# Kernel optimization log

Measured on AMD Instinct MI355X. Metric: run time of the kernel, lower is better.

The kernel has to match this reference:

```python
import jax, jax.numpy as jnp
import numpy as np

N_USER = 60082   # n_fields: size of station/field table
N_STATION = 14695
D = 128
B = 8
K = 32


def setup_inputs() -> dict:
    key = jax.random.key(0)
    ks = jax.random.split(key, 20)
    inp = {
        'user_embedding': jax.random.normal(ks[0], (B, D), jnp.float32),
        'station_embedding': jax.random.normal(ks[1], (N_USER, D), jnp.float32),
        'raw_field_embed': jax.random.normal(ks[2], (N_USER, D), jnp.float32),
        'his_nodes': jax.random.randint(ks[3], (B, K), 0, N_USER),
        'now_nodes': jax.random.randint(ks[4], (B, K), 0, N_USER),
        'user_id': jax.random.randint(ks[5], (B,), 0, N_STATION),
        # learned parameters
        'user_emb_table': jax.random.normal(ks[6], (N_STATION, D), jnp.float32) * 0.02,
        'station_emb_table': jax.random.normal(ks[7], (N_USER, D), jnp.float32) * 0.02,
        'proj_w': jax.random.normal(ks[8], (D, D), jnp.float32) / np.sqrt(D),
        'proj_b': jnp.zeros((D,), jnp.float32),
        'theta': jax.random.uniform(ks[9], (N_STATION, 1), jnp.float32),
        'alpha': jax.random.uniform(ks[10], (N_USER, 1), jnp.float32),
        'w_his1': jax.random.normal(ks[11], (D, D // 2), jnp.float32) / np.sqrt(D),
        'b_his1': jnp.zeros((D // 2,), jnp.float32),
        'w_his2': jax.random.normal(ks[12], (D // 2, D), jnp.float32) / np.sqrt(D // 2),
        'b_his2': jnp.zeros((D,), jnp.float32),
        'w_st': jax.random.normal(ks[13], (D, 1), jnp.float32) / np.sqrt(D),
        'b_st': jnp.zeros((1,), jnp.float32),
        'w_u': jax.random.normal(ks[14], (D, 1), jnp.float32) / np.sqrt(D),
        'b_u': jnp.zeros((1,), jnp.float32),
    }
    return inp


def reference(user_embedding, station_embedding, raw_field_embed,
              user_emb_table, station_emb_table, proj_w, proj_b,
              theta, alpha, w_his1, b_his1, w_his2, b_his2,
              w_st, b_st, w_u, b_u,
              his_nodes, now_nodes, user_id):
    # user_mem_stat: gated mix of dynamic and static user embedding (dropout = eval identity)
    th = theta[user_id]                                    # [B,1]
    user_mem = (1.0 - th) * user_embedding + th * user_emb_table[user_id]  # [B,D]

    # full-table projection, shared across batch (the torch loop recomputes it)
    proj = station_emb_table @ proj_w + proj_b             # [N,D]

    b_idx = jnp.arange(B)[:, None]                         # [B,1]
    beta = jnp.zeros((B, N_USER), user_embedding.dtype)
    beta = beta.at[b_idx, now_nodes].set(1.0)
    beta = beta.at[b_idx, his_nodes].set(1.0)              # use_his=True path

    embed = (1.0 - beta[..., None] * alpha[None]) * proj[None]  # [B,N,D]

    # scatter-add current-node contribution
    now_add = alpha[now_nodes] * station_embedding[now_nodes]  # [B,K,D]
    embed = embed.at[b_idx, now_nodes].add(now_add)

    # history MLP (Linear -> LeakyReLU -> Linear) on gathered raw field embeds
    h = raw_field_embed[his_nodes]                         # [B,K,D]
    h = jax.nn.leaky_relu(h @ w_his1 + b_his1) @ w_his2 + b_his2
    embed = embed.at[b_idx, his_nodes].add(alpha[his_nodes] * h)

    station_out = (embed @ w_st)[..., 0] + b_st[0]         # [B,N]
    user_out = user_mem @ w_u + b_u                        # [B,1]
    return station_out + user_out                          # [B,N]
```

## Files before the change

### kernel.cpp

```cpp
#include <hip/hip_runtime.h>

#define NU 60082
#define NST 14695
#define D 128
#define B 8
#define K 32
#define NSTREAM ((NU + 63) / 64)

__global__ __launch_bounds__(256) void k_fused(
    const float* __restrict__ user_embedding,
    const float* __restrict__ station_embedding,
    const float* __restrict__ raw_field_embed,
    const int* __restrict__ his_nodes,
    const int* __restrict__ now_nodes,
    const int* __restrict__ user_id,
    const float* __restrict__ user_emb_table,
    const float* __restrict__ station_emb_table,
    const float* __restrict__ proj_w,
    const float* __restrict__ proj_b,
    const float* __restrict__ theta,
    const float* __restrict__ alpha,
    const float* __restrict__ w_his1,
    const float* __restrict__ b_his1,
    const float* __restrict__ w_his2,
    const float* __restrict__ b_his2,
    const float* __restrict__ w_st,
    const float* __restrict__ b_st,
    const float* __restrict__ w_u,
    const float* __restrict__ b_u,
    float* __restrict__ out)
{
    const int t = threadIdx.x;

    if (blockIdx.x < B) {
        __shared__ float s_wst[128];
        __shared__ float s_v[128];
        __shared__ float s_v2[64];
        __shared__ float s_rfe[32][128];
        __shared__ int   s_nodes[64];
        __shared__ float s_alpha[64];
        __shared__ float s_vals[64];
        __shared__ float s_sn[64];
        __shared__ float s_c, s_c2, s_uc;
        const int b = blockIdx.x;

        if (t < 32) ((float4*)s_wst)[t] = ((const float4*)w_st)[t];
        if (t >= 64 && t < 128) {
            int j = t - 64;
            s_nodes[j] = (j < K) ? now_nodes[b * K + j] : his_nodes[b * K + (j - K)];
        }
        __syncthreads();

        if (t < 128) {
            float acc = 0.f;
            const float4* pr = (const float4*)(proj_w + t * D);
            #pragma unroll 8
            for (int j = 0; j < 32; ++j) {
                float4 x = pr[j];
                float4 wv = ((float4*)s_wst)[j];
                acc += x.x * wv.x + x.y * wv.y + x.z * wv.z + x.w * wv.w;
            }
            s_v[t] = acc;
        } else if (t < 192) {
            int u = t - 128;
            float acc = 0.f;
            const float4* pr = (const float4*)(w_his2 + u * D);
            #pragma unroll 8
            for (int j = 0; j < 32; ++j) {
                float4 x = pr[j];
                float4 wv = ((float4*)s_wst)[j];
                acc += x.x * wv.x + x.y * wv.y + x.z * wv.z + x.w * wv.w;
            }
            s_v2[u] = acc;
        } else if (t < 224) {
            int l = t - 192;
            float4 x = ((const float4*)proj_b)[l];
            float4 wv = ((float4*)s_wst)[l];
            float p = x.x * wv.x + x.y * wv.y + x.z * wv.z + x.w * wv.w;
            #pragma unroll
            for (int off = 16; off >= 1; off >>= 1) p += __shfl_down(p, off, 32);
            if (l == 0) s_c = p;
        } else {
            int l = t - 224;
            float4 x = ((const float4*)b_his2)[l];
            float4 wv = ((float4*)s_wst)[l];
            float p = x.x * wv.x + x.y * wv.y + x.z * wv.z + x.w * wv.w;
            #pragma unroll
            for (int off = 16; off >= 1; off >>= 1) p += __shfl_down(p, off, 32);
            if (l == 0) s_c2 = p;
        }
        if (t < 32) {
            int uid = user_id[b];
            float th = theta[uid];
            float4 ue = ((const float4*)(user_embedding + b * D))[t];
            float4 ut = ((const float4*)(user_emb_table + (size_t)uid * D))[t];
            float4 wu = ((const float4*)w_u)[t];
            float p = ((1.f - th) * ue.x + th * ut.x) * wu.x
                    + ((1.f - th) * ue.y + th * ut.y) * wu.y
                    + ((1.f - th) * ue.z + th * ut.z) * wu.z
                    + ((1.f - th) * ue.w + th * ut.w) * wu.w;
            #pragma unroll
            for (int off = 16; off >= 1; off >>= 1) p += __shfl_down(p, off, 32);
            if (t == 0) s_uc = p + b_u[0] + b_st[0];
        }
        if (t >= 32 && t < 96) s_alpha[t - 32] = alpha[s_nodes[t - 32]];
        __syncthreads();

        {
            int j = t >> 3, c8 = t & 7;
            int n = s_nodes[32 + j];
            const float4* src = (const float4*)(raw_field_embed + (size_t)n * D);
            #pragma unroll
            for (int i = 0; i < 4; ++i)
                ((float4*)s_rfe[j])[c8 + 8 * i] = src[c8 + 8 * i];
        }
        __syncthreads();

        {
            const int u = t & 63, w = t >> 6;
            const float v2u = s_v2[u];
            const float bias = b_his1[u];
            float h1[8];
            #pragma unroll
            for (int j = 0; j < 8; ++j) h1[j] = bias;
            for (int dd = 0; dd < 128; dd += 8) {
                float wr[8];
                #pragma unroll
                for (int i = 0; i < 8; ++i) wr[i] = w_his1[(dd + i) * 64 + u];
                #pragma unroll
                for (int j = 0; j < 8; ++j) {
                    const float4* rf = (const float4*)&s_rfe[w * 8 + j][dd];
                    float4 a = rf[0], b4 = rf[1];
                    h1[j] += a.x * wr[0] + a.y * wr[1] + a.z * wr[2] + a.w * wr[3]
                           + b4.x * wr[4] + b4.y * wr[5] + b4.z * wr[6] + b4.w * wr[7];
                }
            }
            #pragma unroll
            for (int j = 0; j < 8; ++j) {
                float ha = h1[j] > 0.f ? h1[j] : 0.01f * h1[j];
                float val = ha * v2u;
                #pragma unroll
                for (int off = 32; off >= 1; off >>= 1) val += __shfl_down(val, off, 64);
                if (u == 0)
                    s_vals[32 + w * 8 + j] = s_alpha[32 + w * 8 + j] * (val + s_c2);
            }
        }
        {
            const int u = t & 63, w = t >> 6;
            #pragma unroll
            for (int r = 0; r < 8; ++r) {
                int j = w * 8 + r;
                int n = s_nodes[j];
                const float* se = station_embedding + (size_t)n * D;
                float p = se[u] * s_wst[u] + se[64 + u] * s_wst[64 + u];
                #pragma unroll
                for (int off = 32; off >= 1; off >>= 1) p += __shfl_down(p, off, 64);
                if (u == 0) s_vals[j] = s_alpha[j] * p;
            }
        }
        {
            int node = t >> 2, q = t & 3;
            const float4* sr = (const float4*)(station_emb_table + (size_t)s_nodes[node] * D);
            float p = 0.f;
            #pragma unroll
            for (int i = 0; i < 8; ++i) {
                float4 x = sr[q + 4 * i];
                float4 vv = ((float4*)s_v)[q + 4 * i];
                p += x.x * vv.x + x.y * vv.y + x.z * vv.z + x.w * vv.w;
            }
            p += __shfl_down(p, 2, 4);
            p += __shfl_down(p, 1, 4);
            if (q == 0) s_sn[node] = p + s_c;
        }
        __syncthreads();

        if (t < 64) {
            int n = s_nodes[t];
            bool first = true;
            for (int i = 0; i < t; ++i)
                if (s_nodes[i] == n) { first = false; break; }
            if (first) {
                float sum = 0.f;
                for (int i = 0; i < 64; ++i)
                    if (s_nodes[i] == n) sum += s_vals[i];
                out[(size_t)b * NU + n] = (1.f - s_alpha[t]) * s_sn[t] + s_uc + sum;
            }
        }
    } else {
        __shared__ float st_wst[128];
        __shared__ float st_v[128];
        __shared__ float st_tile[64];
        __shared__ float st_uc[8];
        __shared__ unsigned char st_flag[8 * 64];
        __shared__ float st_c;
        const int sb = blockIdx.x - B;
        const int row0 = sb * 64;

        if (t < 32) ((float4*)st_wst)[t] = ((const float4*)w_st)[t];
        if (t >= 128) ((int*)st_flag)[t - 128] = 0;
        __syncthreads();

        if (t < 128) {
            float acc = 0.f;
            const float4* pr = (const float4*)(proj_w + t * D);
            #pragma unroll 8
            for (int j = 0; j < 32; ++j) {
                float4 x = pr[j];
                float4 wv = ((float4*)st_wst)[j];
                acc += x.x * wv.x + x.y * wv.y + x.z * wv.z + x.w * wv.w;
            }
            st_v[t] = acc;
        } else if (t < 160) {
            int l = t - 128;
            float4 x = ((const float4*)proj_b)[l];
            float4 wv = ((float4*)st_wst)[l];
            float p = x.x * wv.x + x.y * wv.y + x.z * wv.z + x.w * wv.w;
            #pragma unroll
            for (int off = 16; off >= 1; off >>= 1) p += __shfl_down(p, off, 32);
            if (l == 0) st_c = p;
        }
        {
            int n0 = now_nodes[t];
            if ((n0 >> 6) == sb) st_flag[(t >> 5) * 64 + (n0 & 63)] = 1;
            int n1 = his_nodes[t];
            if ((n1 >> 6) == sb) st_flag[(t >> 5) * 64 + (n1 & 63)] = 1;
        }
        {
            int u = t >> 5, l = t & 31;
            int uid = user_id[u];
            float th = theta[uid];
            float4 ue = ((const float4*)(user_embedding + u * D))[l];
            float4 ut = ((const float4*)(user_emb_table + (size_t)uid * D))[l];
            float4 wu = ((const float4*)w_u)[l];
            float p = ((1.f - th) * ue.x + th * ut.x) * wu.x
                    + ((1.f - th) * ue.y + th * ut.y) * wu.y
                    + ((1.f - th) * ue.z + th * ut.z) * wu.z
                    + ((1.f - th) * ue.w + th * ut.w) * wu.w;
            #pragma unroll
            for (int off = 16; off >= 1; off >>= 1) p += __shfl_down(p, off, 32);
            if (l == 0) st_uc[u] = p + b_u[0] + b_st[0];
        }
        __syncthreads();

        const int w    = t >> 6;
        const int lane = t & 63;
        const int half = lane >> 5;
        const int l32  = lane & 31;
        const float4 vv = ((const float4*)st_v)[l32];
        const float  c  = st_c;
        #pragma unroll
        for (int i = 0; i < 8; ++i) {
            int r = i * 8 + w * 2 + half;
            int row = row0 + r;
            float acc = 0.f;
            if (row < NU) {
                float4 x = ((const float4*)(station_emb_table + (size_t)row * D))[l32];
                acc = x.x * vv.x + x.y * vv.y + x.z * vv.z + x.w * vv.w;
            }
            #pragma unroll
            for (int off = 16; off >= 1; off >>= 1) acc += __shfl_down(acc, off, 32);
            if (l32 == 0) st_tile[r] = acc + c;
        }
        __syncthreads();

        const int nl = t & 63;
        const int b0 = t >> 6;
        const int row = row0 + nl;
        if (row < NU) {
            float sv = st_tile[nl];
            if (!st_flag[b0 * 64 + nl])
                out[(size_t)b0 * NU + row] = sv + st_uc[b0];
            if (!st_flag[(b0 + 4) * 64 + nl])
                out[(size_t)(b0 + 4) * NU + row] = sv + st_uc[b0 + 4];
        }
    }
}

extern "C" void kernel_launch(void* const* d_in, const int* in_sizes, int n_in,
                              void* d_out, int out_size, void* d_ws, size_t ws_size,
                              hipStream_t stream) {
    const float* user_embedding    = (const float*)d_in[0];
    const float* station_embedding = (const float*)d_in[1];
    const float* raw_field_embed   = (const float*)d_in[2];
    const int*   his_nodes         = (const int*)d_in[3];
    const int*   now_nodes         = (const int*)d_in[4];
    const int*   user_id           = (const int*)d_in[5];
    const float* user_emb_table    = (const float*)d_in[6];
    const float* station_emb_table = (const float*)d_in[7];
    const float* proj_w            = (const float*)d_in[8];
    const float* proj_b            = (const float*)d_in[9];
    const float* theta             = (const float*)d_in[10];
    const float* alpha             = (const float*)d_in[11];
    const float* w_his1            = (const float*)d_in[12];
    const float* b_his1            = (const float*)d_in[13];
    const float* w_his2            = (const float*)d_in[14];
    const float* b_his2            = (const float*)d_in[15];
    const float* w_st              = (const float*)d_in[16];
    const float* b_st              = (const float*)d_in[17];
    const float* w_u               = (const float*)d_in[18];
    const float* b_u               = (const float*)d_in[19];
    float* out = (float*)d_out;

    hipLaunchKernelGGL(k_fused, dim3(B + NSTREAM), dim3(256), 0, stream,
                       user_embedding, station_embedding, raw_field_embed,
                       his_nodes, now_nodes, user_id, user_emb_table,
                       station_emb_table, proj_w, proj_b, theta, alpha,
                       w_his1, b_his1, w_his2, b_his2,
                       w_st, b_st, w_u, b_u, out);
}
```

Before: 166.3 us.

## Distribute sparse node corrections into owning row-tile blocks instead of per-batch blocks

Removes the eight dedicated per-batch blocks that handled the gathered now/his nodes. Each streaming tile block now collects, via shared-memory atomics, the node entries that fall in its 64-row range and computes their corrections locally, reusing the projected tile value already in shared memory. This removes the long serial critical path of the per-batch blocks (the MLP over 32 history rows), but adds a conditional tail to some tile blocks, redundant global reads of w_his1 per history node, and an extra barrier.

```diff
diff --git a/kernel.cpp b/kernel.cpp
--- a/kernel.cpp
+++ b/kernel.cpp
@@ -5,7 +5,7 @@
 #define D 128
 #define B 8
 #define K 32
-#define NSTREAM ((NU + 63) / 64)
+#define NBLK ((NU + 63) / 64)
 
 __global__ __launch_bounds__(256) void k_fused(
     const float* __restrict__ user_embedding,
@@ -30,248 +30,187 @@
     const float* __restrict__ b_u,
     float* __restrict__ out)
 {
-    const int t = threadIdx.x;
-
-    if (blockIdx.x < B) {
-        __shared__ float s_wst[128];
-        __shared__ float s_v[128];
-        __shared__ float s_v2[64];
-        __shared__ float s_rfe[32][128];
-        __shared__ int   s_nodes[64];
-        __shared__ float s_alpha[64];
-        __shared__ float s_vals[64];
-        __shared__ float s_sn[64];
-        __shared__ float s_c, s_c2, s_uc;
-        const int b = blockIdx.x;
-
-        if (t < 32) ((float4*)s_wst)[t] = ((const float4*)w_st)[t];
-        if (t >= 64 && t < 128) {
-            int j = t - 64;
-            s_nodes[j] = (j < K) ? now_nodes[b * K + j] : his_nodes[b * K + (j - K)];
-        }
-        __syncthreads();
-
-        if (t < 128) {
-            float acc = 0.f;
-            const float4* pr = (const float4*)(proj_w + t * D);
-            #pragma unroll 8
-            for (int j = 0; j < 32; ++j) {
-                float4 x = pr[j];
-                float4 wv = ((float4*)s_wst)[j];
-                acc += x.x * wv.x + x.y * wv.y + x.z * wv.z + x.w * wv.w;
-            }
-            s_v[t] = acc;
-        } else if (t < 192) {
-            int u = t - 128;
-            float acc = 0.f;
-            const float4* pr = (const float4*)(w_his2 + u * D);
-            #pragma unroll 8
-            for (int j = 0; j < 32; ++j) {
-                float4 x = pr[j];
-                float4 wv = ((float4*)s_wst)[j];
-                acc += x.x * wv.x + x.y * wv.y + x.z * wv.z + x.w * wv.w;
-            }
-            s_v2[u] = acc;
-        } else if (t < 224) {
-            int l = t - 192;
-            float4 x = ((const float4*)proj_b)[l];
-            float4 wv = ((float4*)s_wst)[l];
-            float p = x.x * wv.x + x.y * wv.y + x.z * wv.z + x.w * wv.w;
-            #pragma unroll
-            for (int off = 16; off >= 1; off >>= 1) p += __shfl_down(p, off, 32);
-            if (l == 0) s_c = p;
-        } else {
-            int l = t - 224;
-            float4 x = ((const float4*)b_his2)[l];
-            float4 wv = ((float4*)s_wst)[l];
-            float p = x.x * wv.x + x.y * wv.y + x.z * wv.z + x.w * wv.w;
-            #pragma unroll
-            for (int off = 16; off >= 1; off >>= 1) p += __shfl_down(p, off, 32);
-            if (l == 0) s_c2 = p;
-        }
-        if (t < 32) {
-            int uid = user_id[b];
-            float th = theta[uid];
-            float4 ue = ((const float4*)(user_embedding + b * D))[t];
-            float4 ut = ((const float4*)(user_emb_table + (size_t)uid * D))[t];
-            float4 wu = ((const float4*)w_u)[t];
-            float p = ((1.f - th) * ue.x + th * ut.x) * wu.x
-                    + ((1.f - th) * ue.y + th * ut.y) * wu.y
-                    + ((1.f - th) * ue.z + th * ut.z) * wu.z
-                    + ((1.f - th) * ue.w + th * ut.w) * wu.w;
-            #pragma unroll
-            for (int off = 16; off >= 1; off >>= 1) p += __shfl_down(p, off, 32);
-            if (t == 0) s_uc = p + b_u[0] + b_st[0];
-        }
-        if (t >= 32 && t < 96) s_alpha[t - 32] = alpha[s_nodes[t - 32]];
-        __syncthreads();
-
-        {
-            int j = t >> 3, c8 = t & 7;
-            int n = s_nodes[32 + j];
-            const float4* src = (const float4*)(raw_field_embed + (size_t)n * D);
-            #pragma unroll
-            for (int i = 0; i < 4; ++i)
-                ((float4*)s_rfe[j])[c8 + 8 * i] = src[c8 + 8 * i];
-        }
-        __syncthreads();
-
-        {
-            const int u = t & 63, w = t >> 6;
-            const float v2u = s_v2[u];
-            const float bias = b_his1[u];
-            float h1[8];
-            #pragma unroll
-            for (int j = 0; j < 8; ++j) h1[j] = bias;
-            for (int dd = 0; dd < 128; dd += 8) {
-                float wr[8];
-                #pragma unroll
-                for (int i = 0; i < 8; ++i) wr[i] = w_his1[(dd + i) * 64 + u];
-                #pragma unroll
-                for (int j = 0; j < 8; ++j) {
-                    const float4* rf = (const float4*)&s_rfe[w * 8 + j][dd];
-                    float4 a = rf[0], b4 = rf[1];
-                    h1[j] += a.x * wr[0] + a.y * wr[1] + a.z * wr[2] + a.w * wr[3]
-                           + b4.x * wr[4] + b4.y * wr[5] + b4.z * wr[6] + b4.w * wr[7];
-                }
-            }
-            #pragma unroll
-            for (int j = 0; j < 8; ++j) {
-                float ha = h1[j] > 0.f ? h1[j] : 0.01f * h1[j];
-                float val = ha * v2u;
-                #pragma unroll
-                for (int off = 32; off >= 1; off >>= 1) val += __shfl_down(val, off, 64);
-                if (u == 0)
-                    s_vals[32 + w * 8 + j] = s_alpha[32 + w * 8 + j] * (val + s_c2);
-            }
-        }
-        {
-            const int u = t & 63, w = t >> 6;
-            #pragma unroll
-            for (int r = 0; r < 8; ++r) {
-                int j = w * 8 + r;
-                int n = s_nodes[j];
-                const float* se = station_embedding + (size_t)n * D;
-                float p = se[u] * s_wst[u] + se[64 + u] * s_wst[64 + u];
-                #pragma unroll
-                for (int off = 32; off >= 1; off >>= 1) p += __shfl_down(p, off, 64);
-                if (u == 0) s_vals[j] = s_alpha[j] * p;
-            }
-        }
-        {
-            int node = t >> 2, q = t & 3;
-            const float4* sr = (const float4*)(station_emb_table + (size_t)s_nodes[node] * D);
-            float p = 0.f;
-            #pragma unroll
-            for (int i = 0; i < 8; ++i) {
-                float4 x = sr[q + 4 * i];
-                float4 vv = ((float4*)s_v)[q + 4 * i];
-                p += x.x * vv.x + x.y * vv.y + x.z * vv.z + x.w * vv.w;
-            }
-            p += __shfl_down(p, 2, 4);
-            p += __shfl_down(p, 1, 4);
-            if (q == 0) s_sn[node] = p + s_c;
-        }
-        __syncthreads();
-
-        if (t < 64) {
-            int n = s_nodes[t];
-            bool first = true;
-            for (int i = 0; i < t; ++i)
-                if (s_nodes[i] == n) { first = false; break; }
-            if (first) {
-                float sum = 0.f;
-                for (int i = 0; i < 64; ++i)
-                    if (s_nodes[i] == n) sum += s_vals[i];
-                out[(size_t)b * NU + n] = (1.f - s_alpha[t]) * s_sn[t] + s_uc + sum;
-            }
-        }
-    } else {
-        __shared__ float st_wst[128];
-        __shared__ float st_v[128];
-        __shared__ float st_tile[64];
-        __shared__ float st_uc[8];
-        __shared__ unsigned char st_flag[8 * 64];
-        __shared__ float st_c;
-        const int sb = blockIdx.x - B;
-        const int row0 = sb * 64;
-
-        if (t < 32) ((float4*)st_wst)[t] = ((const float4*)w_st)[t];
-        if (t >= 128) ((int*)st_flag)[t - 128] = 0;
-        __syncthreads();
-
-        if (t < 128) {
-            float acc = 0.f;
-            const float4* pr = (const float4*)(proj_w + t * D);
-            #pragma unroll 8
-            for (int j = 0; j < 32; ++j) {
-                float4 x = pr[j];
-                float4 wv = ((float4*)st_wst)[j];
-                acc += x.x * wv.x + x.y * wv.y + x.z * wv.z + x.w * wv.w;
-            }
-            st_v[t] = acc;
-        } else if (t < 160) {
-            int l = t - 128;
-            float4 x = ((const float4*)proj_b)[l];
-            float4 wv = ((float4*)st_wst)[l];
-            float p = x.x * wv.x + x.y * wv.y + x.z * wv.z + x.w * wv.w;
-            #pragma unroll
-            for (int off = 16; off >= 1; off >>= 1) p += __shfl_down(p, off, 32);
-            if (l == 0) st_c = p;
-        }
-        {
-            int n0 = now_nodes[t];
-            if ((n0 >> 6) == sb) st_flag[(t >> 5) * 64 + (n0 & 63)] = 1;
-            int n1 = his_nodes[t];
-            if ((n1 >> 6) == sb) st_flag[(t >> 5) * 64 + (n1 & 63)] = 1;
-        }
-        {
-            int u = t >> 5, l = t & 31;
-            int uid = user_id[u];
-            float th = theta[uid];
-            float4 ue = ((const float4*)(user_embedding + u * D))[l];
-            float4 ut = ((const float4*)(user_emb_table + (size_t)uid * D))[l];
-            float4 wu = ((const float4*)w_u)[l];
-            float p = ((1.f - th) * ue.x + th * ut.x) * wu.x
-                    + ((1.f - th) * ue.y + th * ut.y) * wu.y
-                    + ((1.f - th) * ue.z + th * ut.z) * wu.z
-                    + ((1.f - th) * ue.w + th * ut.w) * wu.w;
-            #pragma unroll
-            for (int off = 16; off >= 1; off >>= 1) p += __shfl_down(p, off, 32);
-            if (l == 0) st_uc[u] = p + b_u[0] + b_st[0];
-        }
-        __syncthreads();
-
-        const int w    = t >> 6;
-        const int lane = t & 63;
-        const int half = lane >> 5;
-        const int l32  = lane & 31;
-        const float4 vv = ((const float4*)st_v)[l32];
-        const float  c  = st_c;
-        #pragma unroll
-        for (int i = 0; i < 8; ++i) {
-            int r = i * 8 + w * 2 + half;
-            int row = row0 + r;
-            float acc = 0.f;
-            if (row < NU) {
-                float4 x = ((const float4*)(station_emb_table + (size_t)row * D))[l32];
-                acc = x.x * vv.x + x.y * vv.y + x.z * vv.z + x.w * vv.w;
-            }
-            #pragma unroll
-            for (int off = 16; off >= 1; off >>= 1) acc += __shfl_down(acc, off, 32);
-            if (l32 == 0) st_tile[r] = acc + c;
-        }
-        __syncthreads();
-
+    __shared__ float s_wst[128];
+    __shared__ float s_v[128];
+    __shared__ float s_v2[64];
+    __shared__ float s_tile[64];
+    __shared__ float s_uc[8];
+    __shared__ unsigned char s_flag[8 * 64];
+    __shared__ short s_lslot[512];
+    __shared__ int   s_lnode[512];
+    __shared__ float s_lval[512];
+    __shared__ int   s_cnt, s_hcnt;
+    __shared__ float s_c, s_c2;
+
+    const int t  = threadIdx.x;
+    const int sb = blockIdx.x;
+    const int row0 = sb * 64;
+
+    if (t < 32) ((float4*)s_wst)[t] = ((const float4*)w_st)[t];
+    if (t >= 64 && t < 192) ((int*)s_flag)[t - 64] = 0;
+    if (t == 192) s_cnt = 0;
+    if (t == 193) s_hcnt = 0;
+    __syncthreads();
+
+    if (t < 128) {
+        float acc = 0.f;
+        const float4* pr = (const float4*)(proj_w + t * D);
+        #pragma unroll 8
+        for (int j = 0; j < 32; ++j) {
+            float4 x = pr[j];
+            float4 wv = ((float4*)s_wst)[j];
+            acc += x.x * wv.x + x.y * wv.y + x.z * wv.z + x.w * wv.w;
+        }
+        s_v[t] = acc;
+    } else if (t < 160) {
+        int l = t - 128;
+        float4 x = ((const float4*)proj_b)[l];
+        float4 wv = ((float4*)s_wst)[l];
+        float p = x.x * wv.x + x.y * wv.y + x.z * wv.z + x.w * wv.w;
+        #pragma unroll
+        for (int off = 16; off >= 1; off >>= 1) p += __shfl_down(p, off, 32);
+        if (l == 0) s_c = p;
+    } else if (t < 192) {
+        int l = t - 160;
+        float4 x = ((const float4*)b_his2)[l];
+        float4 wv = ((float4*)s_wst)[l];
+        float p = x.x * wv.x + x.y * wv.y + x.z * wv.z + x.w * wv.w;
+        #pragma unroll
+        for (int off = 16; off >= 1; off >>= 1) p += __shfl_down(p, off, 32);
+        if (l == 0) s_c2 = p;
+    }
+
+    {
+        int n0 = now_nodes[t];
+        if ((n0 >> 6) == sb) {
+            s_flag[(t >> 5) * 64 + (n0 & 63)] = 1;
+            int i = atomicAdd(&s_cnt, 1);
+            s_lslot[i] = (short)t;
+            s_lnode[i] = n0;
+        }
+        int n1 = his_nodes[t];
+        if ((n1 >> 6) == sb) {
+            s_flag[(t >> 5) * 64 + (n1 & 63)] = 1;
+            int i = atomicAdd(&s_cnt, 1);
+            s_lslot[i] = (short)(256 + t);
+            s_lnode[i] = n1;
+            atomicAdd(&s_hcnt, 1);
+        }
+    }
+    {
+        int u = t >> 5, l = t & 31;
+        int uid = user_id[u];
+        float th = theta[uid];
+        float4 ue = ((const float4*)(user_embedding + u * D))[l];
+        float4 ut = ((const float4*)(user_emb_table + (size_t)uid * D))[l];
+        float4 wu = ((const float4*)w_u)[l];
+        float p = ((1.f - th) * ue.x + th * ut.x) * wu.x
+                + ((1.f - th) * ue.y + th * ut.y) * wu.y
+                + ((1.f - th) * ue.z + th * ut.z) * wu.z
+                + ((1.f - th) * ue.w + th * ut.w) * wu.w;
+        #pragma unroll
+        for (int off = 16; off >= 1; off >>= 1) p += __shfl_down(p, off, 32);
+        if (l == 0) s_uc[u] = p + b_u[0] + b_st[0];
+    }
+    __syncthreads();
+
+    const int cnt  = s_cnt;
+    const int hcnt = s_hcnt;
+
+    const int w    = t >> 6;
+    const int lane = t & 63;
+    const int half = lane >> 5;
+    const int l32  = lane & 31;
+    const float4 vv = ((const float4*)s_v)[l32];
+    const float  c  = s_c;
+    #pragma unroll
+    for (int i = 0; i < 8; ++i) {
+        int r = i * 8 + w * 2 + half;
+        int row = row0 + r;
+        float acc = 0.f;
+        if (row < NU) {
+            float4 x = ((const float4*)(station_emb_table + (size_t)row * D))[l32];
+            acc = x.x * vv.x + x.y * vv.y + x.z * vv.z + x.w * vv.w;
+        }
+        #pragma unroll
+        for (int off = 16; off >= 1; off >>= 1) acc += __shfl_down(acc, off, 32);
+        if (l32 == 0) s_tile[r] = acc + c;
+    }
+    __syncthreads();
+
+    {
         const int nl = t & 63;
         const int b0 = t >> 6;
         const int row = row0 + nl;
         if (row < NU) {
-            float sv = st_tile[nl];
-            if (!st_flag[b0 * 64 + nl])
-                out[(size_t)b0 * NU + row] = sv + st_uc[b0];
-            if (!st_flag[(b0 + 4) * 64 + nl])
-                out[(size_t)(b0 + 4) * NU + row] = sv + st_uc[b0 + 4];
+            float sv = s_tile[nl];
+            if (!s_flag[b0 * 64 + nl])
+                out[(size_t)b0 * NU + row] = sv + s_uc[b0];
+            if (!s_flag[(b0 + 4) * 64 + nl])
+                out[(size_t)(b0 + 4) * NU + row] = sv + s_uc[b0 + 4];
+        }
+    }
+
+    if (cnt > 0) {
+        if (hcnt > 0) {
+            int row = t >> 2, q = t & 3;
+            const float4* wr = (const float4*)(w_his2 + row * D);
+            float p = 0.f;
+            #pragma unroll
+            for (int i = 0; i < 8; ++i) {
+                float4 x = wr[q + 4 * i];
+                float4 wv = ((float4*)s_wst)[q + 4 * i];
+                p += x.x * wv.x + x.y * wv.y + x.z * wv.z + x.w * wv.w;
+            }
+            p += __shfl_down(p, 2, 4);
+            p += __shfl_down(p, 1, 4);
+            if (q == 0) s_v2[row] = p;
+        }
+        __syncthreads();
+
+        for (int i = w; i < cnt; i += 4) {
+            int slot = s_lslot[i];
+            int n = s_lnode[i];
+            float val;
+            if (slot < 256) {
+                const float* se = station_embedding + (size_t)n * D;
+                float p = se[lane] * s_wst[lane] + se[64 + lane] * s_wst[64 + lane];
+                #pragma unroll
+                for (int off = 32; off >= 1; off >>= 1) p += __shfl_down(p, off, 64);
+                val = alpha[n] * p;
+            } else {
+                const float4* rf = (const float4*)(raw_field_embed + (size_t)n * D);
+                float h1 = b_his1[lane];
+                #pragma unroll 8
+                for (int j = 0; j < 32; ++j) {
+                    float4 r = rf[j];
+                    h1 += r.x * w_his1[(4 * j + 0) * 64 + lane]
+                        + r.y * w_his1[(4 * j + 1) * 64 + lane]
+                        + r.z * w_his1[(4 * j + 2) * 64 + lane]
+                        + r.w * w_his1[(4 * j + 3) * 64 + lane];
+                }
+                float ha = h1 > 0.f ? h1 : 0.01f * h1;
+                float p = ha * s_v2[lane];
+                #pragma unroll
+                for (int off = 32; off >= 1; off >>= 1) p += __shfl_down(p, off, 64);
+                val = alpha[n] * (p + s_c2);
+            }
+            if (lane == 0) s_lval[i] = val;
+        }
+        __syncthreads();
+
+        if (t < cnt) {
+            int n = s_lnode[t];
+            int b = (s_lslot[t] & 255) >> 5;
+            bool first = true;
+            for (int i = 0; i < t; ++i)
+                if (s_lnode[i] == n && ((s_lslot[i] & 255) >> 5) == b) { first = false; break; }
+            if (first) {
+                float sum = 0.f;
+                for (int i = 0; i < cnt; ++i)
+                    if (s_lnode[i] == n && ((s_lslot[i] & 255) >> 5) == b) sum += s_lval[i];
+                out[(size_t)b * NU + n] = (1.f - alpha[n]) * s_tile[n - row0] + s_uc[b] + sum;
+            }
         }
     }
 }
@@ -301,7 +240,7 @@
     const float* b_u               = (const float*)d_in[19];
     float* out = (float*)d_out;
 
-    hipLaunchKernelGGL(k_fused, dim3(B + NSTREAM), dim3(256), 0, stream,
+    hipLaunchKernelGGL(k_fused, dim3(NBLK), dim3(256), 0, stream,
                        user_embedding, station_embedding, raw_field_embed,
                        his_nodes, now_nodes, user_id, user_emb_table,
                        station_emb_table, proj_w, proj_b, theta, alpha,
```

Result: faster. 157.5 us (-5.3%).
